# Performance work log

Measured on AMD Instinct MI355X. Metric: run time of the kernel, lower is better.

The kernel has to match this reference:

```python
import jax, jax.numpy as jnp
import numpy as np
from jax.scipy.linalg import expm

B = 131072
ROT_DIM = 32   # rot_latent_dim
TRZ_DIM = 32   # tranz_latent_dim
W = 128        # MLP_hidden_layer_width


def setup_inputs() -> dict:
    key = jax.random.key(0)
    ks = jax.random.split(key, 13)
    def g(k, shape, scale):
        return jax.random.normal(k, shape, dtype=jnp.float32) * scale
    return {
        "y": g(ks[0], (B, ROT_DIM + TRZ_DIM), 1.0),
        # omega MLP: 32 -> 128 -> 128 -> 9
        "ow0": g(ks[1], (W, ROT_DIM), 1.0 / np.sqrt(ROT_DIM)),
        "ob0": g(ks[2], (W,), 0.01),
        "ow1": g(ks[3], (W, W), 1.0 / np.sqrt(W)),
        "ob1": g(ks[4], (W,), 0.01),
        "ow2": g(ks[5], (9, W), 1.0 / np.sqrt(W)),
        "ob2": g(ks[6], (9,), 0.01),
        # tranz MLP: 32 -> 128 -> 128 -> 3
        "tw0": g(ks[7], (W, TRZ_DIM), 1.0 / np.sqrt(TRZ_DIM)),
        "tb0": g(ks[8], (W,), 0.01),
        "tw1": g(ks[9], (W, W), 1.0 / np.sqrt(W)),
        "tb1": g(ks[10], (W,), 0.01),
        "tw2": g(ks[11], (3, W), 1.0 / np.sqrt(W)),
        "tb2": g(ks[12], (3,), 0.01),
    }


def _mlp(x, weights, biases):
    # eqx.nn.Linear: W @ x + b; ReLU on all but last layer
    n = len(weights)
    for i, (w, b) in enumerate(zip(weights, biases)):
        x = jnp.einsum("bi,oi->bo", x, w) + b
        if i + 1 < n:
            x = jax.nn.relu(x)
    return x


def reference(y, ow0, ob0, ow1, ob1, ow2, ob2, tw0, tb0, tw1, tb1, tw2, tb2):
    x = y[:, :ROT_DIM]            # dynamic_slice(0, rot_latent_dim)
    z = y[:, ROT_DIM:ROT_DIM + TRZ_DIM]
    omega = _mlp(x, [ow0, ow1, ow2], [ob0, ob1, ob2])       # [B, 9]
    # exp_omega: reshape to 3x3, matrix exponential, flatten back
    rot = jax.vmap(expm)(omega.reshape(B, 3, 3)).reshape(B, 9)
    trz = _mlp(z, [tw0, tw1, tw2], [tb0, tb1, tb2])          # [B, 3]
    return jnp.concatenate([rot, trz], axis=1)               # [B, 12]
```

## Files before the change

kernel.cpp:

```cpp
#include <hip/hip_runtime.h>
#include <hip/hip_bf16.h>
#include <stdint.h>

typedef short  short8  __attribute__((ext_vector_type(8)));
typedef float  floatx4 __attribute__((ext_vector_type(4)));

#define WS_W0_ROT   0
#define WS_W0_TRZ   8192
#define WS_W1_ROT   16384
#define WS_W1_TRZ   49152
#define WS_W2_ROT   81920
#define WS_W2_TRZ   86016
#define WS_BIAS     90112

__device__ __forceinline__ unsigned short f2bf_rne(float f) {
    union { float f; unsigned u; } v; v.f = f;
    unsigned r = v.u + 0x7fffu + ((v.u >> 16) & 1u);
    return (unsigned short)(r >> 16);
}

__global__ void prep_kernel(const float* __restrict__ ow0, const float* __restrict__ ow1,
                            const float* __restrict__ ow2, const float* __restrict__ tw0,
                            const float* __restrict__ tw1, const float* __restrict__ tw2,
                            const float* __restrict__ ob0, const float* __restrict__ ob1,
                            const float* __restrict__ ob2, const float* __restrict__ tb0,
                            const float* __restrict__ tb1, const float* __restrict__ tb2,
                            unsigned char* __restrict__ ws)
{
    int t = blockIdx.x * 256 + threadIdx.x;
    unsigned short* w16 = (unsigned short*)ws;
    if (t < 4096) {
        w16[t] = f2bf_rne(ow0[t]);
    } else if (t < 8192) {
        w16[t] = f2bf_rne(tw0[t - 4096]);
    } else if (t < 24576) {
        int i = t - 8192; int n = i >> 7, p = i & 127;
        w16[t] = f2bf_rne(ow1[n * 128 + ((p & 7) << 4) + (p >> 3)]);
    } else if (t < 40960) {
        int i = t - 24576; int n = i >> 7, p = i & 127;
        w16[t] = f2bf_rne(tw1[n * 128 + ((p & 7) << 4) + (p >> 3)]);
    } else if (t < 43008) {
        int i = t - 40960; int n = i >> 7, p = i & 127;
        w16[t] = (n < 9) ? f2bf_rne(ow2[n * 128 + ((p & 7) << 4) + (p >> 3)]) : (unsigned short)0;
    } else if (t < 45056) {
        int i = t - 43008; int n = i >> 7, p = i & 127;
        w16[t] = (n < 3) ? f2bf_rne(tw2[n * 128 + ((p & 7) << 4) + (p >> 3)]) : (unsigned short)0;
    } else if (t < 45600) {
        int i = t - 45056;
        float v;
        if      (i < 128) v = ob0[i];
        else if (i < 256) v = ob1[i - 128];
        else if (i < 272) v = (i - 256 < 9) ? ob2[i - 256] : 0.0f;
        else if (i < 400) v = tb0[i - 272];
        else if (i < 528) v = tb1[i - 400];
        else              v = (i - 528 < 3) ? tb2[i - 528] : 0.0f;
        ((float*)(ws + WS_BIAS))[i] = v;
    }
}

__device__ __forceinline__ floatx4 mfma16(short8 a, short8 b, floatx4 c) {
    return __builtin_amdgcn_mfma_f32_16x16x32_bf16(a, b, c, 0, 0, 0);
}

__device__ __forceinline__ double pack4(floatx4 a) {
    union { unsigned u[2]; double d; } r;
    union { __hip_bfloat162 b2; unsigned u; } c;
    c.b2 = __float22bfloat162_rn(make_float2(a[0], a[1])); r.u[0] = c.u;
    c.b2 = __float22bfloat162_rn(make_float2(a[2], a[3])); r.u[1] = c.u;
    return r.d;
}

__device__ __forceinline__ void write_h_b64(char* hb, int q, int ln, int f,
                                            const floatx4* acc) {
    #pragma unroll
    for (int r = 0; r < 4; ++r) {
        const int m = q * 4 + r;
        union { unsigned u[2]; double d; } pk;
        union { __hip_bfloat162 b2; unsigned u; } c;
        c.b2 = __float22bfloat162_rn(make_float2(fmaxf(acc[0][r], 0.0f), fmaxf(acc[1][r], 0.0f)));
        pk.u[0] = c.u;
        c.b2 = __float22bfloat162_rn(make_float2(fmaxf(acc[2][r], 0.0f), fmaxf(acc[3][r], 0.0f)));
        pk.u[1] = c.u;
        *(double*)(hb + m * 256 + ((ln ^ m) << 4) + (f << 3)) = pk.d;
    }
}

__device__ __forceinline__ void read_a_b128(const char* hb, int q, int ln, short8* a) {
    #pragma unroll
    for (int s2 = 0; s2 < 4; ++s2) {
        const int cp = (s2 * 4 + q) ^ ln;
        a[s2] = *(const short8*)(hb + ln * 256 + cp * 16);
    }
}

__device__ __forceinline__ void mat3mul(float* C, const float* A, const float* B) {
    #pragma unroll
    for (int i = 0; i < 3; ++i)
        #pragma unroll
        for (int j = 0; j < 3; ++j)
            C[i*3+j] = A[i*3+0]*B[0+j] + A[i*3+1]*B[3+j] + A[i*3+2]*B[6+j];
}

__launch_bounds__(256, 3)
__global__ void fused_main(const float* __restrict__ y,
                           const unsigned char* __restrict__ ws,
                           float* __restrict__ out)
{
    __shared__ __align__(16) unsigned char lds_h0[2][4096];
    __shared__ __align__(16) unsigned char lds_h1[2][4096];
    __shared__ __align__(16) unsigned char lds_yx[4][1280];
    __shared__ __align__(16) float lds_stage[128 * 12];

    const int tid  = threadIdx.x;
    const int wv   = tid >> 6;
    const int lane = tid & 63;
    const int ln   = lane & 15;
    const int q    = lane >> 4;
    const int mlp  = wv >> 1;
    const int f    = wv & 1;
    const int wgbase = blockIdx.x * 128;

    const int W0_OFF = mlp ? WS_W0_TRZ : WS_W0_ROT;
    const int W1_OFF = mlp ? WS_W1_TRZ : WS_W1_ROT;
    const int W2_OFF = mlp ? WS_W2_TRZ : WS_W2_ROT;
    const float* bias = (const float*)(ws + WS_BIAS) + (mlp ? 272 : 0);

    const int r8 = lane >> 3, c8 = lane & 7;
    const float* ygbase = y + (size_t)wgbase * 64 + mlp * 32 + c8 * 4;

    floatx4 curA = *(const floatx4*)(ygbase + (size_t)r8 * 64);
    floatx4 curB = *(const floatx4*)(ygbase + (size_t)(r8 + 8) * 64);

    short8 bw0[4], bw1[16], bw2[4];
    #pragma unroll
    for (int j = 0; j < 4; ++j)
        bw0[j] = *(const short8*)(ws + W0_OFF + (((f * 4 + j) * 16 + ln) * 32 + q * 8) * 2);
    #pragma unroll
    for (int j = 0; j < 4; ++j) {
        #pragma unroll
        for (int s2 = 0; s2 < 4; ++s2)
            bw1[j * 4 + s2] = *(const short8*)(ws + W1_OFF + (((f * 4 + j) * 16 + ln) * 128 + s2 * 32 + q * 8) * 2);
    }
    #pragma unroll
    for (int s2 = 0; s2 < 4; ++s2)
        bw2[s2] = *(const short8*)(ws + W2_OFF + (ln * 128 + s2 * 32 + q * 8) * 2);

    float b0v[4], b1v[4];
    #pragma unroll
    for (int j = 0; j < 4; ++j) {
        b0v[j] = bias[(f * 4 + j) * 16 + ln];
        b1v[j] = bias[128 + (f * 4 + j) * 16 + ln];
    }
    const float b2v = bias[256 + ln];

    char* hb0 = (char*)lds_h0[mlp];
    char* hb1 = (char*)lds_h1[mlp];
    char* yxb = (char*)lds_yx[wv];
    const int cb     = mlp ? 9 : 0;
    const int nvalid = mlp ? 3 : 9;

    #pragma unroll 1
    for (int g = 0; g < 8; ++g) {
        *(double*)(yxb + r8 * 80 + c8 * 8)       = pack4(curA);
        *(double*)(yxb + (r8 + 8) * 80 + c8 * 8) = pack4(curB);

        if (g < 7) {
            curA = *(const floatx4*)(ygbase + (size_t)((g + 1) * 16 + r8) * 64);
            curB = *(const floatx4*)(ygbase + (size_t)((g + 1) * 16 + r8 + 8) * 64);
        }

        __builtin_amdgcn_s_waitcnt(0xC07F);
        short8 a0 = *(const short8*)(yxb + ln * 80 + q * 16);

        floatx4 acc[4];
        #pragma unroll
        for (int j = 0; j < 4; ++j) {
            floatx4 c = {b0v[j], b0v[j], b0v[j], b0v[j]};
            acc[j] = mfma16(a0, bw0[j], c);
        }
        write_h_b64(hb0, q, ln, f, acc);

        __syncthreads();

        short8 a1[4];
        read_a_b128(hb0, q, ln, a1);

        #pragma unroll
        for (int j = 0; j < 4; ++j) {
            floatx4 c = {b1v[j], b1v[j], b1v[j], b1v[j]};
            #pragma unroll
            for (int s2 = 0; s2 < 4; ++s2)
                c = mfma16(a1[s2], bw1[j * 4 + s2], c);
            acc[j] = c;
        }
        write_h_b64(hb1, q, ln, f, acc);

        __syncthreads();

        short8 a2[4];
        read_a_b128(hb1, q, ln, a2);

        floatx4 acc2 = {b2v, b2v, b2v, b2v};
        #pragma unroll
        for (int s2 = 0; s2 < 4; ++s2)
            acc2 = mfma16(a2[s2], bw2[s2], acc2);

        if (f == 0 && ln < nvalid) {
            const int rl = g * 16 + q * 4;
            #pragma unroll
            for (int r = 0; r < 4; ++r)
                lds_stage[(rl + r) * 12 + cb + ln] = acc2[r];
        }
    }

    __syncthreads();

    if (tid < 128) {
        float* st = &lds_stage[tid * 12];
        floatx4 m0 = *(floatx4*)(st);
        floatx4 m1 = *(floatx4*)(st + 4);
        floatx4 m2 = *(floatx4*)(st + 8);
        float M[9] = {m0[0], m0[1], m0[2], m0[3], m1[0], m1[1], m1[2], m1[3], m2[0]};
        const float tz0 = m2[1], tz1 = m2[2], tz2 = m2[3];

        float r0 = fabsf(M[0]) + fabsf(M[1]) + fabsf(M[2]);
        float r1 = fabsf(M[3]) + fabsf(M[4]) + fabsf(M[5]);
        float r2 = fabsf(M[6]) + fabsf(M[7]) + fabsf(M[8]);
        float nrm = fmaxf(r0, fmaxf(r1, r2));
        int e; (void)frexpf(nrm, &e);
        int s = e + 1;
        if (s < 0) s = 0;
        if (s > 24) s = 24;
        float sc;
        { union { unsigned u; float fv; } cv; cv.u = (unsigned)(127 - s) << 23; sc = cv.fv; }
        #pragma unroll
        for (int i = 0; i < 9; ++i) M[i] *= sc;

        float Rm[9];
        #pragma unroll
        for (int i = 0; i < 9; ++i) Rm[i] = 0.0f;
        Rm[0] = Rm[4] = Rm[8] = 1.0f;
        #pragma unroll
        for (int j = 10; j >= 1; --j) {
            float T[9]; mat3mul(T, M, Rm);
            const float inv = 1.0f / (float)j;
            #pragma unroll
            for (int i = 0; i < 9; ++i) Rm[i] = T[i] * inv;
            Rm[0] += 1.0f; Rm[4] += 1.0f; Rm[8] += 1.0f;
        }
        for (int it = 0; it < s; ++it) {
            float T[9]; mat3mul(T, Rm, Rm);
            #pragma unroll
            for (int i = 0; i < 9; ++i) Rm[i] = T[i];
        }

        floatx4 o0 = {Rm[0], Rm[1], Rm[2], Rm[3]};
        floatx4 o1 = {Rm[4], Rm[5], Rm[6], Rm[7]};
        floatx4 o2 = {Rm[8], tz0, tz1, tz2};
        *(floatx4*)(st)     = o0;
        *(floatx4*)(st + 4) = o1;
        *(floatx4*)(st + 8) = o2;
    }

    __syncthreads();

    {
        float* ob = out + (size_t)wgbase * 12;
        floatx4 v = *(floatx4*)&lds_stage[tid * 4];
        *(floatx4*)(ob + tid * 4) = v;
        if (tid < 128) {
            floatx4 v2 = *(floatx4*)&lds_stage[(256 + tid) * 4];
            *(floatx4*)(ob + (256 + tid) * 4) = v2;
        }
    }
}

extern "C" void kernel_launch(void* const* d_in, const int* in_sizes, int n_in,
                              void* d_out, int out_size, void* d_ws, size_t ws_size,
                              hipStream_t stream)
{
    const float* y = (const float*)d_in[0];
    prep_kernel<<<179, 256, 0, stream>>>(
        (const float*)d_in[1], (const float*)d_in[3], (const float*)d_in[5],
        (const float*)d_in[7], (const float*)d_in[9], (const float*)d_in[11],
        (const float*)d_in[2], (const float*)d_in[4], (const float*)d_in[6],
        (const float*)d_in[8], (const float*)d_in[10], (const float*)d_in[12],
        (unsigned char*)d_ws);
    fused_main<<<1024, 256, 0, stream>>>(y, (const unsigned char*)d_ws, (float*)d_out);
}
```

Before: 145.3 us.

## Give each wave a full MLP to remove per-layer block barriers

```diff
diff --git a/kernel.cpp b/kernel.cpp
--- a/kernel.cpp
+++ b/kernel.cpp
@@ -70,7 +70,7 @@
     return r.d;
 }
 
-__device__ __forceinline__ void write_h_b64(char* hb, int q, int ln, int f,
+__device__ __forceinline__ void write_h_b64(char* hb, int q, int ln, int p,
                                             const floatx4* acc) {
     #pragma unroll
     for (int r = 0; r < 4; ++r) {
@@ -81,7 +81,7 @@
         pk.u[0] = c.u;
         c.b2 = __float22bfloat162_rn(make_float2(fmaxf(acc[2][r], 0.0f), fmaxf(acc[3][r], 0.0f)));
         pk.u[1] = c.u;
-        *(double*)(hb + m * 256 + ((ln ^ m) << 4) + (f << 3)) = pk.d;
+        *(double*)(hb + m * 256 + ((ln ^ m) << 4) + (p << 3)) = pk.d;
     }
 }
 
@@ -101,14 +101,13 @@
             C[i*3+j] = A[i*3+0]*B[0+j] + A[i*3+1]*B[3+j] + A[i*3+2]*B[6+j];
 }
 
-__launch_bounds__(256, 3)
+__launch_bounds__(128, 2)
 __global__ void fused_main(const float* __restrict__ y,
                            const unsigned char* __restrict__ ws,
                            float* __restrict__ out)
 {
-    __shared__ __align__(16) unsigned char lds_h0[2][4096];
-    __shared__ __align__(16) unsigned char lds_h1[2][4096];
-    __shared__ __align__(16) unsigned char lds_yx[4][1280];
+    __shared__ __align__(16) unsigned char lds_h[2][4096];
+    __shared__ __align__(16) unsigned char lds_yx[2][1280];
     __shared__ __align__(16) float lds_stage[128 * 12];
 
     const int tid  = threadIdx.x;
@@ -116,8 +115,7 @@
     const int lane = tid & 63;
     const int ln   = lane & 15;
     const int q    = lane >> 4;
-    const int mlp  = wv >> 1;
-    const int f    = wv & 1;
+    const int mlp  = wv;
     const int wgbase = blockIdx.x * 128;
 
     const int W0_OFF = mlp ? WS_W0_TRZ : WS_W0_ROT;
@@ -131,30 +129,29 @@
     floatx4 curA = *(const floatx4*)(ygbase + (size_t)r8 * 64);
     floatx4 curB = *(const floatx4*)(ygbase + (size_t)(r8 + 8) * 64);
 
-    short8 bw0[4], bw1[16], bw2[4];
-    #pragma unroll
-    for (int j = 0; j < 4; ++j)
-        bw0[j] = *(const short8*)(ws + W0_OFF + (((f * 4 + j) * 16 + ln) * 32 + q * 8) * 2);
-    #pragma unroll
-    for (int j = 0; j < 4; ++j) {
+    short8 bw0[8], bw1[32], bw2[4];
+    #pragma unroll
+    for (int nt = 0; nt < 8; ++nt)
+        bw0[nt] = *(const short8*)(ws + W0_OFF + ((nt * 16 + ln) * 32 + q * 8) * 2);
+    #pragma unroll
+    for (int nt = 0; nt < 8; ++nt) {
         #pragma unroll
         for (int s2 = 0; s2 < 4; ++s2)
-            bw1[j * 4 + s2] = *(const short8*)(ws + W1_OFF + (((f * 4 + j) * 16 + ln) * 128 + s2 * 32 + q * 8) * 2);
+            bw1[nt * 4 + s2] = *(const short8*)(ws + W1_OFF + ((nt * 16 + ln) * 128 + s2 * 32 + q * 8) * 2);
     }
     #pragma unroll
     for (int s2 = 0; s2 < 4; ++s2)
         bw2[s2] = *(const short8*)(ws + W2_OFF + (ln * 128 + s2 * 32 + q * 8) * 2);
 
-    float b0v[4], b1v[4];
-    #pragma unroll
-    for (int j = 0; j < 4; ++j) {
-        b0v[j] = bias[(f * 4 + j) * 16 + ln];
-        b1v[j] = bias[128 + (f * 4 + j) * 16 + ln];
+    float b0v[8], b1v[8];
+    #pragma unroll
+    for (int nt = 0; nt < 8; ++nt) {
+        b0v[nt] = bias[nt * 16 + ln];
+        b1v[nt] = bias[128 + nt * 16 + ln];
     }
     const float b2v = bias[256 + ln];
 
-    char* hb0 = (char*)lds_h0[mlp];
-    char* hb1 = (char*)lds_h1[mlp];
+    char* hb  = (char*)lds_h[wv];
     char* yxb = (char*)lds_yx[wv];
     const int cb     = mlp ? 9 : 0;
     const int nvalid = mlp ? 3 : 9;
@@ -172,40 +169,45 @@
         __builtin_amdgcn_s_waitcnt(0xC07F);
         short8 a0 = *(const short8*)(yxb + ln * 80 + q * 16);
 
-        floatx4 acc[4];
-        #pragma unroll
-        for (int j = 0; j < 4; ++j) {
-            floatx4 c = {b0v[j], b0v[j], b0v[j], b0v[j]};
-            acc[j] = mfma16(a0, bw0[j], c);
-        }
-        write_h_b64(hb0, q, ln, f, acc);
-
-        __syncthreads();
+        #pragma unroll
+        for (int p = 0; p < 2; ++p) {
+            floatx4 acc[4];
+            #pragma unroll
+            for (int j = 0; j < 4; ++j) {
+                const float b = b0v[p * 4 + j];
+                floatx4 c = {b, b, b, b};
+                acc[j] = mfma16(a0, bw0[p * 4 + j], c);
+            }
+            write_h_b64(hb, q, ln, p, acc);
+        }
 
         short8 a1[4];
-        read_a_b128(hb0, q, ln, a1);
-
-        #pragma unroll
-        for (int j = 0; j < 4; ++j) {
-            floatx4 c = {b1v[j], b1v[j], b1v[j], b1v[j]};
-            #pragma unroll
-            for (int s2 = 0; s2 < 4; ++s2)
-                c = mfma16(a1[s2], bw1[j * 4 + s2], c);
-            acc[j] = c;
-        }
-        write_h_b64(hb1, q, ln, f, acc);
-
-        __syncthreads();
+        read_a_b128(hb, q, ln, a1);
+
+        #pragma unroll
+        for (int p = 0; p < 2; ++p) {
+            floatx4 acc[4];
+            #pragma unroll
+            for (int j = 0; j < 4; ++j) {
+                const float b = b1v[p * 4 + j];
+                floatx4 c = {b, b, b, b};
+                #pragma unroll
+                for (int s2 = 0; s2 < 4; ++s2)
+                    c = mfma16(a1[s2], bw1[(p * 4 + j) * 4 + s2], c);
+                acc[j] = c;
+            }
+            write_h_b64(hb, q, ln, p, acc);
+        }
 
         short8 a2[4];
-        read_a_b128(hb1, q, ln, a2);
+        read_a_b128(hb, q, ln, a2);
 
         floatx4 acc2 = {b2v, b2v, b2v, b2v};
         #pragma unroll
         for (int s2 = 0; s2 < 4; ++s2)
             acc2 = mfma16(a2[s2], bw2[s2], acc2);
 
-        if (f == 0 && ln < nvalid) {
+        if (ln < nvalid) {
             const int rl = g * 16 + q * 4;
             #pragma unroll
             for (int r = 0; r < 4; ++r)
@@ -215,7 +217,7 @@
 
     __syncthreads();
 
-    if (tid < 128) {
+    {
         float* st = &lds_stage[tid * 12];
         floatx4 m0 = *(floatx4*)(st);
         floatx4 m1 = *(floatx4*)(st + 4);
@@ -266,11 +268,11 @@
 
     {
         float* ob = out + (size_t)wgbase * 12;
-        floatx4 v = *(floatx4*)&lds_stage[tid * 4];
-        *(floatx4*)(ob + tid * 4) = v;
-        if (tid < 128) {
-            floatx4 v2 = *(floatx4*)&lds_stage[(256 + tid) * 4];
-            *(floatx4*)(ob + (256 + tid) * 4) = v2;
+        #pragma unroll
+        for (int k = 0; k < 3; ++k) {
+            const int j = k * 128 + tid;
+            floatx4 v = *(floatx4*)&lds_stage[j * 4];
+            *(floatx4*)(ob + j * 4) = v;
         }
     }
 }
@@ -286,5 +288,5 @@
         (const float*)d_in[2], (const float*)d_in[4], (const float*)d_in[6],
         (const float*)d_in[8], (const float*)d_in[10], (const float*)d_in[12],
         (unsigned char*)d_ws);
-    fused_main<<<1024, 256, 0, stream>>>(y, (const unsigned char*)d_ws, (float*)d_out);
-}
+    fused_main<<<1024, 128, 0, stream>>>(y, (const unsigned char*)d_ws, (float*)d_out);
+}
```

After: 157.2 us. +8.2%, slower.
